# Kernel optimization log

Measured on AMD Instinct MI355X. Metric: run time of the kernel, lower is better.

The kernel has to match this reference:

```python
import jax, jax.numpy as jnp
import numpy as np

NUM_HEADS = 16

def setup_inputs() -> dict:
    key = jax.random.key(0)
    ks = jax.random.split(key, 5)
    d_model = 1024
    x = jax.random.normal(ks[0], (2, 2048, d_model), dtype=jnp.float32)
    # xavier-uniform-like scale for square [d_model, d_model] weights
    lim = float(np.sqrt(6.0 / (d_model + d_model)))
    def w(k):
        return jax.random.uniform(k, (d_model, d_model), dtype=jnp.float32, minval=-lim, maxval=lim)
    return {"x": x, "Wq": w(ks[1]), "Wk": w(ks[2]), "Wv": w(ks[3]), "Wo": w(ks[4])}

def reference(x, Wq, Wk, Wv, Wo):
    B, S, D = x.shape
    H = NUM_HEADS
    dk = D // H
    # project: torch does x @ W.T
    def split_heads(t):
        return t.reshape(B, S, H, dk).transpose(0, 2, 1, 3)  # [B,H,S,dk]
    q = split_heads(x @ Wq.T)
    k = split_heads(x @ Wk.T)
    v = split_heads(x @ Wv.T)
    scores = jnp.einsum('bhqd,bhkd->bhqk', q, k) / jnp.sqrt(jnp.float32(dk))
    causal = jnp.tril(jnp.ones((S, S), dtype=bool))  # True where attended
    scores = jnp.where(causal[None, None], scores, -jnp.inf)
    probs = jax.nn.softmax(scores, axis=-1)
    out = jnp.einsum('bhqk,bhkd->bhqd', probs, v)  # [B,H,S,dk]
    out = out.transpose(0, 2, 1, 3).reshape(B, S, D)
    return out @ Wo.T
```

## Files before the change

kernel.cpp:

```cpp
#include <hip/hip_runtime.h>
#include <stdint.h>

#define BATCH  2
#define SEQ    2048
#define DMODEL 1024
#define NHEADS 16
#define DKH    64
#define MTOT   (BATCH*SEQ)
#define VSTR   (SEQ + 32)

typedef unsigned short u16;
typedef __bf16 bf16x8 __attribute__((ext_vector_type(8)));
typedef float  f32x4  __attribute__((ext_vector_type(4)));

extern "C" __device__ float __ocml_native_exp2_f32(float);

__device__ __forceinline__ u16 f2bf(float f) {
  union { float f; uint32_t u; } v; v.f = f;
  uint32_t u = v.u;
  return (u16)((u + 0x7FFFu + ((u >> 16) & 1u)) >> 16);
}
__device__ __forceinline__ float bf2f(u16 h) {
  union { uint32_t u; float f; } v; v.u = (uint32_t)h << 16; return v.f;
}

__device__ __forceinline__ void gld_lds16(const void* g, void* l) {
  __builtin_amdgcn_global_load_lds(
      (__attribute__((address_space(1))) void*)g,
      (__attribute__((address_space(3))) void*)l, 16, 0, 0);
}

__global__ void cvt_f32_bf16(const float* __restrict__ src, u16* __restrict__ dst) {
  size_t i = ((size_t)blockIdx.x * 256 + threadIdx.x) * 4;
  float4 f = *(const float4*)(src + i);
  ushort4 o;
  o.x = f2bf(f.x); o.y = f2bf(f.y); o.z = f2bf(f.z); o.w = f2bf(f.w);
  *(ushort4*)(dst + i) = o;
}
__global__ void cvt_w(const float* __restrict__ a, const float* __restrict__ b,
                      const float* __restrict__ c, const float* __restrict__ d,
                      u16* __restrict__ dst) {
  const float* srcs[4] = {a, b, c, d};
  const float* s = srcs[blockIdx.y];
  size_t i = ((size_t)blockIdx.x * 256 + threadIdx.x) * 4;
  float4 f = *(const float4*)(s + i);
  ushort4 o;
  o.x = f2bf(f.x); o.y = f2bf(f.y); o.z = f2bf(f.z); o.w = f2bf(f.w);
  *(ushort4*)(dst + (size_t)blockIdx.y * (DMODEL*DMODEL) + i) = o;
}

__device__ __forceinline__ void gemm_core(const u16* A, const u16* W,
                                          int m0, int n0, f32x4 acc[4][4],
                                          u16* lA, u16* lB) {
  const int tid  = threadIdx.x;
  const int lane = tid & 63;
  const int lrow = lane & 15;
  const int quad = lane >> 4;
  const int wave = tid >> 6;
  const int wm   = (wave & 1) * 64;
  const int wn   = (wave >> 1) * 64;
  const int sx   = lrow & 7;

  for (int k0 = 0; k0 < DMODEL; k0 += 64) {
    #pragma unroll
    for (int r = 0; r < 4; ++r) {
      int off  = r * 4096 + tid * 16;
      int row  = off >> 7;
      int c16  = (off >> 4) & 7;
      int colb = (c16 ^ (row & 7)) << 4;
      gld_lds16((const char*)A + ((size_t)(m0 + row) * DMODEL + k0) * 2 + colb,
                (char*)lA + off);
      gld_lds16((const char*)W + ((size_t)(n0 + row) * DMODEL + k0) * 2 + colb,
                (char*)lB + off);
    }
    __syncthreads();
    #pragma unroll
    for (int ks = 0; ks < 2; ++ks) {
      bf16x8 a[4], b[4];
      const int ce = ((ks << 2) | quad);
      #pragma unroll
      for (int i = 0; i < 4; ++i)
        a[i] = *(const bf16x8*)(lA + (wm + i*16 + lrow) * 64 + ((ce ^ sx) << 3));
      #pragma unroll
      for (int i = 0; i < 4; ++i)
        b[i] = *(const bf16x8*)(lB + (wn + i*16 + lrow) * 64 + ((ce ^ sx) << 3));
      #pragma unroll
      for (int i = 0; i < 4; ++i)
        #pragma unroll
        for (int j = 0; j < 4; ++j)
          acc[i][j] = __builtin_amdgcn_mfma_f32_16x16x32_bf16(a[i], b[j], acc[i][j], 0, 0, 0);
    }
    __syncthreads();
  }
}

__global__ __launch_bounds__(256) void gemm_qkv(
    const u16* __restrict__ xb, const u16* __restrict__ wq,
    const u16* __restrict__ wk, const u16* __restrict__ wv,
    u16* __restrict__ q, u16* __restrict__ k, u16* __restrict__ v, float qscale) {
  __shared__ __align__(16) u16 lA[128 * 64];
  __shared__ __align__(16) u16 lB[128 * 64];
  const int z = blockIdx.z;
  const u16* W = (z == 0) ? wq : (z == 1) ? wk : wv;
  u16* out     = (z == 0) ? q  : (z == 1) ? k  : v;
  const float scale = (z == 0) ? qscale : 1.0f;
  const int m0 = blockIdx.x * 128, n0 = blockIdx.y * 128;
  f32x4 acc[4][4] = {};
  gemm_core(xb, W, m0, n0, acc, lA, lB);

  const int lane = threadIdx.x & 63;
  const int wave = threadIdx.x >> 6;
  const int wm = (wave & 1) * 64, wn = (wave >> 1) * 64;
  const int rb = (lane >> 4) * 4, cb = lane & 15;
  if (z == 2) {
    #pragma unroll
    for (int i = 0; i < 4; ++i)
      #pragma unroll
      for (int j = 0; j < 4; ++j) {
        int row0 = m0 + wm + i*16 + rb;
        int col  = n0 + wn + j*16 + cb;
        int b_ = row0 >> 11, s0 = row0 & 2047;
        int h_ = col >> 6,  d_ = col & 63;
        ushort4 pk;
        pk.x = f2bf(acc[i][j][0]); pk.y = f2bf(acc[i][j][1]);
        pk.z = f2bf(acc[i][j][2]); pk.w = f2bf(acc[i][j][3]);
        *(ushort4*)&out[((size_t)(b_*NHEADS + h_) * DKH + d_) * VSTR + s0] = pk;
      }
  } else {
    #pragma unroll
    for (int i = 0; i < 4; ++i)
      #pragma unroll
      for (int j = 0; j < 4; ++j)
        #pragma unroll
        for (int r = 0; r < 4; ++r) {
          int row = m0 + wm + i*16 + rb + r;
          int col = n0 + wn + j*16 + cb;
          int b_ = row >> 11, s_ = row & 2047;
          int h_ = col >> 6,  d_ = col & 63;
          out[(((size_t)(b_*NHEADS + h_) * SEQ + s_) << 6) + d_] =
              f2bf(acc[i][j][r] * scale);
        }
  }
}

__global__ __launch_bounds__(256) void gemm_out(
    const u16* __restrict__ ab, const u16* __restrict__ wo, float* __restrict__ out) {
  __shared__ __align__(16) u16 lA[128 * 64];
  __shared__ __align__(16) u16 lB[128 * 64];
  const int m0 = blockIdx.x * 128, n0 = blockIdx.y * 128;
  f32x4 acc[4][4] = {};
  gemm_core(ab, wo, m0, n0, acc, lA, lB);

  const int lane = threadIdx.x & 63;
  const int wave = threadIdx.x >> 6;
  const int wm = (wave & 1) * 64, wn = (wave >> 1) * 64;
  const int rb = (lane >> 4) * 4, cb = lane & 15;
  #pragma unroll
  for (int i = 0; i < 4; ++i)
    #pragma unroll
    for (int j = 0; j < 4; ++j)
      #pragma unroll
      for (int r = 0; r < 4; ++r)
        out[(size_t)(m0 + wm + i*16 + rb + r) * DMODEL + (n0 + wn + j*16 + cb)]
            = acc[i][j][r];
}

#define PSTR 68
__device__ const uint8_t JT[60] = {
  124,125,120,121,116,117,112,113,108,109,104,105,100,101,96,97,92,93,
  88,84,80,76,72,68,64,60,56,52,48,44,
  89,40, 85,36, 81,32, 126,77,28, 122,73,24, 118,69,20, 114,65,16,
  110,61,12, 106,57,8, 102,53,4, 98,49,0
};

__global__ __launch_bounds__(64, 2) void attn(
    const u16* __restrict__ Q, const u16* __restrict__ K,
    const u16* __restrict__ V, u16* __restrict__ O,
    u16* __restrict__ po, float* __restrict__ pl) {
  __shared__ __align__(16) u16 Ps[4][16 * PSTR];

  const int lane = threadIdx.x & 63;
  const int lrow = lane & 15;
  const int quad = lane >> 4;
  const int kq   = quad * 8;

  const int g  = blockIdx.x >> 5;
  const int bh = blockIdx.x & 31;
  const int e  = JT[g];
  const int p  = e >> 2, c = e & 3;
  const int lo = c * 12;
  const int hi = (p + 1 < lo + 12) ? p + 1 : lo + 12;

  const u16* Qg = Q + (size_t)bh * SEQ * DKH;
  const u16* Kg = K + (size_t)bh * SEQ * DKH;
  const u16* Vg = V + (size_t)bh * DKH * VSTR;

  bf16x8 aq[4][2];
  #pragma unroll
  for (int i = 0; i < 4; ++i)
    #pragma unroll
    for (int ks = 0; ks < 2; ++ks)
      aq[i][ks] = *(const bf16x8*)(Qg + (size_t)(64*p + 16*i + lrow) * DKH + ks*32 + kq);

  f32x4 o_acc[4][4] = {};
  float l_acc[4][4] = {};

  const u16* kbase = Kg + (size_t)lrow * DKH + kq;
  const u16* vbase = Vg + (size_t)lrow * VSTR + kq;

  for (int t = lo; t < hi; ++t) {
    bf16x8 kf[2][4], vf[2][4];
    #pragma unroll
    for (int ks = 0; ks < 2; ++ks)
      #pragma unroll
      for (int j = 0; j < 4; ++j) {
        kf[ks][j] = *(const bf16x8*)(kbase + (size_t)t*64*DKH + j*16*DKH + ks*32);
        vf[ks][j] = *(const bf16x8*)(vbase + t*64 + (size_t)j*16*VSTR + ks*32);
      }
    const bool mk = (t == p);

    #pragma unroll
    for (int i = 0; i < 4; ++i) {
      f32x4 s_acc[4] = {};
      #pragma unroll
      for (int ks = 0; ks < 2; ++ks)
        #pragma unroll
        for (int j = 0; j < 4; ++j)
          s_acc[j] = __builtin_amdgcn_mfma_f32_16x16x32_bf16(aq[i][ks], kf[ks][j], s_acc[j], 0, 0, 0);

      if (mk) {
        const int qloc = 16*i + quad*4;
        #pragma unroll
        for (int j = 0; j < 4; ++j) {
          int kloc = j*16 + lrow;
          #pragma unroll
          for (int r = 0; r < 4; ++r)
            if (kloc > qloc + r) s_acc[j][r] = -1e30f;
        }
      }

      #pragma unroll
      for (int j = 0; j < 4; ++j)
        #pragma unroll
        for (int r = 0; r < 4; ++r) {
          float pv = __ocml_native_exp2_f32(s_acc[j][r]);
          l_acc[i][r] += pv;
          union { float f; uint32_t u; } cv; cv.f = pv;
          Ps[i][(quad*4 + r) * PSTR + j*16 + lrow] = (u16)(cv.u >> 16);
        }

      #pragma unroll
      for (int ks = 0; ks < 2; ++ks) {
        bf16x8 ap = *(const bf16x8*)(&Ps[i][lrow * PSTR + ks*32 + kq]);
        #pragma unroll
        for (int j = 0; j < 4; ++j)
          o_acc[i][j] = __builtin_amdgcn_mfma_f32_16x16x32_bf16(ap, vf[ks][j], o_acc[i][j], 0, 0, 0);
      }
    }
  }

  float lr[4][4];
  #pragma unroll
  for (int i = 0; i < 4; ++i)
    #pragma unroll
    for (int r = 0; r < 4; ++r) {
      float sm = l_acc[i][r];
      #pragma unroll
      for (int d = 1; d < 16; d <<= 1) sm += __shfl_xor(sm, d, 64);
      lr[i][r] = sm;
    }

  if (p <= 11) {
    const int h = bh & 15, b_ = bh >> 4;
    #pragma unroll
    for (int i = 0; i < 4; ++i)
      #pragma unroll
      for (int j = 0; j < 4; ++j)
        #pragma unroll
        for (int r = 0; r < 4; ++r) {
          int sg = 64*p + 16*i + quad*4 + r;
          O[(size_t)(b_ * SEQ + sg) * DMODEL + h * DKH + j*16 + lrow]
              = f2bf(o_acc[i][j][r] / lr[i][r]);
        }
  } else {
    const int base = (p < 24) ? (p - 12) * 2 : 24 + (p - 24) * 3;
    const int slot = (base + c) * 32 + bh;
    #pragma unroll
    for (int i = 0; i < 4; ++i) {
      #pragma unroll
      for (int j = 0; j < 4; ++j) {
        ushort4 pk;
        pk.x = f2bf(o_acc[i][j][0]); pk.y = f2bf(o_acc[i][j][1]);
        pk.z = f2bf(o_acc[i][j][2]); pk.w = f2bf(o_acc[i][j][3]);
        *(ushort4*)&po[(size_t)slot * 4096 + (j*16 + lrow) * 64 + 16*i + quad*4] = pk;
      }
      if (lrow == 0)
        #pragma unroll
        for (int r = 0; r < 4; ++r)
          pl[slot * 64 + 16*i + quad*4 + r] = lr[i][r];
    }
  }
}

__global__ __launch_bounds__(256) void combine(
    const u16* __restrict__ po, const float* __restrict__ pl, u16* __restrict__ ab) {
  __shared__ u16 Ls[64][68];
  const int b  = blockIdx.x;
  const int p  = 12 + (b >> 5);
  const int bh = b & 31;
  const int t  = threadIdx.x;
  const int col = t >> 2;
  const int r0  = (t & 3) * 16;
  const int base = (p < 24) ? (p - 12) * 2 : 24 + (p - 24) * 3;
  const int nc   = (p < 24) ? 2 : 3;

  float acc[16], lsum[16];
  {
    const size_t s0 = (size_t)(base * 32 + bh);
    const u16*   q0 = po + s0 * 4096 + col * 64 + r0;
    const float* l0 = pl + s0 * 64 + r0;
    #pragma unroll
    for (int q4 = 0; q4 < 4; ++q4) {
      ushort4 a = *(const ushort4*)(q0 + q4 * 4);
      ushort4 c2 = *(const ushort4*)(q0 + 32 * 4096 + q4 * 4);
      acc[q4*4+0] = bf2f(a.x) + bf2f(c2.x);
      acc[q4*4+1] = bf2f(a.y) + bf2f(c2.y);
      acc[q4*4+2] = bf2f(a.z) + bf2f(c2.z);
      acc[q4*4+3] = bf2f(a.w) + bf2f(c2.w);
      float4 f = *(const float4*)(l0 + q4 * 4);
      float4 g = *(const float4*)(l0 + 32 * 64 + q4 * 4);
      lsum[q4*4+0] = f.x + g.x; lsum[q4*4+1] = f.y + g.y;
      lsum[q4*4+2] = f.z + g.z; lsum[q4*4+3] = f.w + g.w;
    }
    if (nc == 3) {
      const u16*   q2 = q0 + (size_t)64 * 4096;
      const float* l2 = l0 + (size_t)64 * 64;
      #pragma unroll
      for (int q4 = 0; q4 < 4; ++q4) {
        ushort4 a = *(const ushort4*)(q2 + q4 * 4);
        acc[q4*4+0] += bf2f(a.x); acc[q4*4+1] += bf2f(a.y);
        acc[q4*4+2] += bf2f(a.z); acc[q4*4+3] += bf2f(a.w);
        float4 f = *(const float4*)(l2 + q4 * 4);
        lsum[q4*4+0] += f.x; lsum[q4*4+1] += f.y;
        lsum[q4*4+2] += f.z; lsum[q4*4+3] += f.w;
      }
    }
  }
  #pragma unroll
  for (int q = 0; q < 16; ++q)
    Ls[r0 + q][col] = f2bf(acc[q] / lsum[q]);
  __syncthreads();

  const int row = t >> 2;
  const int c0  = (t & 3) * 16;
  const int b_ = bh >> 4, h = bh & 15;
  u16* dst = ab + (size_t)(b_ * SEQ + 64 * p + row) * DMODEL + h * DKH + c0;
  #pragma unroll
  for (int q = 0; q < 16; q += 4)
    *(ushort4*)(dst + q) = *(const ushort4*)&Ls[row][c0 + q];
}

extern "C" void kernel_launch(void* const* d_in, const int* in_sizes, int n_in,
                              void* d_out, int out_size, void* d_ws, size_t ws_size,
                              hipStream_t stream) {
  const float* x  = (const float*)d_in[0];
  const float* Wq = (const float*)d_in[1];
  const float* Wk = (const float*)d_in[2];
  const float* Wv = (const float*)d_in[3];
  const float* Wo = (const float*)d_in[4];
  float* out = (float*)d_out;

  u16* xb  = (u16*)d_ws;
  u16* wqb = xb  + (size_t)MTOT * DMODEL;
  u16* wkb = wqb + (size_t)DMODEL * DMODEL;
  u16* wvb = wkb + (size_t)DMODEL * DMODEL;
  u16* wob = wvb + (size_t)DMODEL * DMODEL;
  u16* qb  = wob + (size_t)DMODEL * DMODEL;
  u16* kb  = qb  + (size_t)MTOT * DMODEL;
  u16* vb  = kb  + (size_t)MTOT * DMODEL;
  u16* ab  = vb  + (size_t)BATCH * NHEADS * DKH * VSTR;
  u16* po  = xb;
  float* pl = (float*)(po + (size_t)1536 * 4096);

  cvt_f32_bf16<<<MTOT * DMODEL / 1024, 256, 0, stream>>>(x, xb);
  cvt_w<<<dim3(DMODEL * DMODEL / 1024, 4), 256, 0, stream>>>(Wq, Wk, Wv, Wo, wqb);

  const float qscale = 0.125f * 1.44269504088896340736f;
  gemm_qkv<<<dim3(MTOT / 128, DMODEL / 128, 3), 256, 0, stream>>>(
      xb, wqb, wkb, wvb, qb, kb, vb, qscale);

  attn<<<1920, 64, 0, stream>>>(qb, kb, vb, ab, po, pl);
  combine<<<640, 256, 0, stream>>>(po, pl, ab);

  gemm_out<<<dim3(MTOT / 128, DMODEL / 128), 256, 0, stream>>>(ab, wob, out);
}
```

Baseline: 190.5 us.

## Replace LDS-staged GEMM tiles with per-wave direct global loads into MFMA

Both projection GEMMs drop the shared-memory staging (global_load_lds, swizzle, block barriers). Each wave now loads its own A and W fragments straight from global memory into registers and issues MFMAs on them, using smaller per-wave tiles (64x64 for QKV, 32x64 for the output GEMM) with more blocks and occupancy hints. This removes LDS traffic and __syncthreads stalls. In exchange, waves in a block no longer share loads, so global/L2 traffic rises and the fragment loads are strided row reads.

```diff
diff --git a/kernel.cpp b/kernel.cpp
--- a/kernel.cpp
+++ b/kernel.cpp
@@ -22,12 +22,6 @@
 }
 __device__ __forceinline__ float bf2f(u16 h) {
   union { uint32_t u; float f; } v; v.u = (uint32_t)h << 16; return v.f;
-}
-
-__device__ __forceinline__ void gld_lds16(const void* g, void* l) {
-  __builtin_amdgcn_global_load_lds(
-      (__attribute__((address_space(1))) void*)g,
-      (__attribute__((address_space(3))) void*)l, 16, 0, 0);
 }
 
 __global__ void cvt_f32_bf16(const float* __restrict__ src, u16* __restrict__ dst) {
@@ -49,82 +43,63 @@
   *(ushort4*)(dst + (size_t)blockIdx.y * (DMODEL*DMODEL) + i) = o;
 }
 
-__device__ __forceinline__ void gemm_core(const u16* A, const u16* W,
-                                          int m0, int n0, f32x4 acc[4][4],
-                                          u16* lA, u16* lB) {
-  const int tid  = threadIdx.x;
-  const int lane = tid & 63;
+__device__ __forceinline__ void gemm_wave64(const u16* __restrict__ A,
+                                            const u16* __restrict__ W,
+                                            int m0, int n0, f32x4 acc[4][4]) {
+  const int lane = threadIdx.x & 63;
   const int lrow = lane & 15;
-  const int quad = lane >> 4;
-  const int wave = tid >> 6;
-  const int wm   = (wave & 1) * 64;
-  const int wn   = (wave >> 1) * 64;
-  const int sx   = lrow & 7;
-
+  const int kq   = (lane >> 4) * 8;
+  const u16* ab = A + (size_t)(m0 + lrow) * DMODEL + kq;
+  const u16* wb = W + (size_t)(n0 + lrow) * DMODEL + kq;
   for (int k0 = 0; k0 < DMODEL; k0 += 64) {
-    #pragma unroll
-    for (int r = 0; r < 4; ++r) {
-      int off  = r * 4096 + tid * 16;
-      int row  = off >> 7;
-      int c16  = (off >> 4) & 7;
-      int colb = (c16 ^ (row & 7)) << 4;
-      gld_lds16((const char*)A + ((size_t)(m0 + row) * DMODEL + k0) * 2 + colb,
-                (char*)lA + off);
-      gld_lds16((const char*)W + ((size_t)(n0 + row) * DMODEL + k0) * 2 + colb,
-                (char*)lB + off);
-    }
-    __syncthreads();
-    #pragma unroll
-    for (int ks = 0; ks < 2; ++ks) {
-      bf16x8 a[4], b[4];
-      const int ce = ((ks << 2) | quad);
+    bf16x8 a[4][2], b[4][2];
+    #pragma unroll
+    for (int i = 0; i < 4; ++i)
+      #pragma unroll
+      for (int ks = 0; ks < 2; ++ks) {
+        a[i][ks] = *(const bf16x8*)(ab + (size_t)i*16*DMODEL + k0 + ks*32);
+        b[i][ks] = *(const bf16x8*)(wb + (size_t)i*16*DMODEL + k0 + ks*32);
+      }
+    #pragma unroll
+    for (int ks = 0; ks < 2; ++ks)
       #pragma unroll
       for (int i = 0; i < 4; ++i)
-        a[i] = *(const bf16x8*)(lA + (wm + i*16 + lrow) * 64 + ((ce ^ sx) << 3));
-      #pragma unroll
-      for (int i = 0; i < 4; ++i)
-        b[i] = *(const bf16x8*)(lB + (wn + i*16 + lrow) * 64 + ((ce ^ sx) << 3));
-      #pragma unroll
-      for (int i = 0; i < 4; ++i)
         #pragma unroll
         for (int j = 0; j < 4; ++j)
-          acc[i][j] = __builtin_amdgcn_mfma_f32_16x16x32_bf16(a[i], b[j], acc[i][j], 0, 0, 0);
-    }
-    __syncthreads();
-  }
-}
-
-__global__ __launch_bounds__(256) void gemm_qkv(
+          acc[i][j] = __builtin_amdgcn_mfma_f32_16x16x32_bf16(a[i][ks], b[j][ks], acc[i][j], 0, 0, 0);
+  }
+}
+
+__global__ __launch_bounds__(256, 3) void gemm_qkv(
     const u16* __restrict__ xb, const u16* __restrict__ wq,
     const u16* __restrict__ wk, const u16* __restrict__ wv,
     u16* __restrict__ q, u16* __restrict__ k, u16* __restrict__ v, float qscale) {
-  __shared__ __align__(16) u16 lA[128 * 64];
-  __shared__ __align__(16) u16 lB[128 * 64];
   const int z = blockIdx.z;
   const u16* W = (z == 0) ? wq : (z == 1) ? wk : wv;
   u16* out     = (z == 0) ? q  : (z == 1) ? k  : v;
   const float scale = (z == 0) ? qscale : 1.0f;
-  const int m0 = blockIdx.x * 128, n0 = blockIdx.y * 128;
+  const int wave = threadIdx.x >> 6;
+  const int m0 = (blockIdx.x * 4 + wave) * 64;
+  const int n0 = blockIdx.y * 64;
+
   f32x4 acc[4][4] = {};
-  gemm_core(xb, W, m0, n0, acc, lA, lB);
+  gemm_wave64(xb, W, m0, n0, acc);
 
   const int lane = threadIdx.x & 63;
-  const int wave = threadIdx.x >> 6;
-  const int wm = (wave & 1) * 64, wn = (wave >> 1) * 64;
   const int rb = (lane >> 4) * 4, cb = lane & 15;
+  const int h = n0 >> 6;
   if (z == 2) {
     #pragma unroll
     for (int i = 0; i < 4; ++i)
       #pragma unroll
       for (int j = 0; j < 4; ++j) {
-        int row0 = m0 + wm + i*16 + rb;
-        int col  = n0 + wn + j*16 + cb;
+        int row0 = m0 + i*16 + rb;
         int b_ = row0 >> 11, s0 = row0 & 2047;
-        int h_ = col >> 6,  d_ = col & 63;
+        int d_ = j*16 + cb;
         ushort4 pk;
         pk.x = f2bf(acc[i][j][0]); pk.y = f2bf(acc[i][j][1]);
         pk.z = f2bf(acc[i][j][2]); pk.w = f2bf(acc[i][j][3]);
-        *(ushort4*)&out[((size_t)(b_*NHEADS + h_) * DKH + d_) * VSTR + s0] = pk;
+        *(ushort4*)&out[((size_t)(b_*NHEADS + h) * DKH + d_) * VSTR + s0] = pk;
       }
   } else {
     #pragma unroll
@@ -133,35 +108,55 @@
       for (int j = 0; j < 4; ++j)
         #pragma unroll
         for (int r = 0; r < 4; ++r) {
-          int row = m0 + wm + i*16 + rb + r;
-          int col = n0 + wn + j*16 + cb;
+          int row = m0 + i*16 + rb + r;
           int b_ = row >> 11, s_ = row & 2047;
-          int h_ = col >> 6,  d_ = col & 63;
-          out[(((size_t)(b_*NHEADS + h_) * SEQ + s_) << 6) + d_] =
+          int d_ = j*16 + cb;
+          out[(((size_t)(b_*NHEADS + h) * SEQ + s_) << 6) + d_] =
               f2bf(acc[i][j][r] * scale);
         }
   }
 }
 
-__global__ __launch_bounds__(256) void gemm_out(
+__global__ __launch_bounds__(256, 4) void gemm_out(
     const u16* __restrict__ ab, const u16* __restrict__ wo, float* __restrict__ out) {
-  __shared__ __align__(16) u16 lA[128 * 64];
-  __shared__ __align__(16) u16 lB[128 * 64];
-  const int m0 = blockIdx.x * 128, n0 = blockIdx.y * 128;
-  f32x4 acc[4][4] = {};
-  gemm_core(ab, wo, m0, n0, acc, lA, lB);
-
+  const int wave = threadIdx.x >> 6;
+  const int m0 = (blockIdx.x * 4 + wave) * 32;
+  const int n0 = blockIdx.y * 64;
   const int lane = threadIdx.x & 63;
-  const int wave = threadIdx.x >> 6;
-  const int wm = (wave & 1) * 64, wn = (wave >> 1) * 64;
+  const int lrow = lane & 15;
+  const int kq   = (lane >> 4) * 8;
+
+  f32x4 acc[2][4] = {};
+  const u16* arow = ab + (size_t)(m0 + lrow) * DMODEL + kq;
+  const u16* wrow = wo + (size_t)(n0 + lrow) * DMODEL + kq;
+  for (int k0 = 0; k0 < DMODEL; k0 += 64) {
+    bf16x8 a[2][2], b[4][2];
+    #pragma unroll
+    for (int ks = 0; ks < 2; ++ks) {
+      #pragma unroll
+      for (int i = 0; i < 2; ++i)
+        a[i][ks] = *(const bf16x8*)(arow + (size_t)i*16*DMODEL + k0 + ks*32);
+      #pragma unroll
+      for (int j = 0; j < 4; ++j)
+        b[j][ks] = *(const bf16x8*)(wrow + (size_t)j*16*DMODEL + k0 + ks*32);
+    }
+    #pragma unroll
+    for (int ks = 0; ks < 2; ++ks)
+      #pragma unroll
+      for (int i = 0; i < 2; ++i)
+        #pragma unroll
+        for (int j = 0; j < 4; ++j)
+          acc[i][j] = __builtin_amdgcn_mfma_f32_16x16x32_bf16(a[i][ks], b[j][ks], acc[i][j], 0, 0, 0);
+  }
+
   const int rb = (lane >> 4) * 4, cb = lane & 15;
   #pragma unroll
-  for (int i = 0; i < 4; ++i)
+  for (int i = 0; i < 2; ++i)
     #pragma unroll
     for (int j = 0; j < 4; ++j)
       #pragma unroll
       for (int r = 0; r < 4; ++r)
-        out[(size_t)(m0 + wm + i*16 + rb + r) * DMODEL + (n0 + wn + j*16 + cb)]
+        out[(size_t)(m0 + i*16 + rb + r) * DMODEL + (n0 + j*16 + cb)]
             = acc[i][j][r];
 }
 
@@ -386,11 +381,11 @@
   cvt_w<<<dim3(DMODEL * DMODEL / 1024, 4), 256, 0, stream>>>(Wq, Wk, Wv, Wo, wqb);
 
   const float qscale = 0.125f * 1.44269504088896340736f;
-  gemm_qkv<<<dim3(MTOT / 128, DMODEL / 128, 3), 256, 0, stream>>>(
+  gemm_qkv<<<dim3(16, 16, 3), 256, 0, stream>>>(
       xb, wqb, wkb, wvb, qb, kb, vb, qscale);
 
   attn<<<1920, 64, 0, stream>>>(qb, kb, vb, ab, po, pl);
   combine<<<640, 256, 0, stream>>>(po, pl, ab);
 
-  gemm_out<<<dim3(MTOT / 128, DMODEL / 128), 256, 0, stream>>>(ab, wob, out);
-}
+  gemm_out<<<dim3(32, 16), 256, 0, stream>>>(ab, wob, out);
+}
```

Result: slower. 264.0 us (+38.6%).
